# Performance work log

Measured on AMD Instinct MI355X. Metric: run time of the kernel, lower is better.

Reference implementation:

```python
import jax, jax.numpy as jnp
import numpy as np

H = 128
L = 3
G = 1024  # num graphs
BN_EPS = 1e-5


def _bn(h, gamma, beta):
    # BatchNorm1d in training mode: biased batch statistics over dim 0
    mu = jnp.mean(h, axis=0)
    var = jnp.var(h, axis=0)
    return (h - mu) * jax.lax.rsqrt(var + BN_EPS) * gamma + beta


def setup_inputs() -> dict:
    key = jax.random.key(0)
    ks = jax.random.split(key, 24)
    N, E, ND, ED = 100000, 1600000, 64, 16
    s = lambda k, shp: jax.random.normal(k, shp, dtype=jnp.float32) * 0.05
    inp = {
        "x": jax.random.normal(ks[0], (N, ND), dtype=jnp.float32),
        "edge_attr": jax.random.normal(ks[1], (E, ED), dtype=jnp.float32),
        "edge_index": jax.random.randint(ks[2], (2, E), 0, N, dtype=jnp.int32),
        "batch": jnp.sort(jax.random.randint(ks[3], (N,), 0, G, dtype=jnp.int32)),
        # embeddings
        "node_W": s(ks[4], (ND, H)), "node_b": jnp.zeros((H,), jnp.float32),
        "edge_W": s(ks[5], (ED, H)), "edge_b": jnp.zeros((H,), jnp.float32),
        # per-layer GINE MLP params (stacked over L layers)
        "W1s": s(ks[6], (L, H, 2 * H)), "b1s": jnp.zeros((L, 2 * H), jnp.float32),
        "g1s": jnp.ones((L, 2 * H), jnp.float32), "be1s": jnp.zeros((L, 2 * H), jnp.float32),
        "W2s": s(ks[7], (L, 2 * H, H)), "b2s": jnp.zeros((L, H), jnp.float32),
        "epss": jnp.zeros((L,), jnp.float32),  # train_eps=True, init 0
        # post-conv batchnorms
        "bn_g": jnp.ones((L, H), jnp.float32), "bn_b": jnp.zeros((L, H), jnp.float32),
        # readout
        "ro_W1": s(ks[8], (H, H)), "ro_b1": jnp.zeros((H,), jnp.float32),
        "ro_W2": s(ks[9], (H, H)), "ro_b2": jnp.zeros((H,), jnp.float32),
    }
    return inp


def reference(x, edge_attr, node_W, node_b, edge_W, edge_b, W1s, b1s, g1s, be1s,
              W2s, b2s, epss, bn_g, bn_b, ro_W1, ro_b1, ro_W2, ro_b2,
              edge_index, batch):
    N = x.shape[0]
    src, dst = edge_index[0], edge_index[1]
    h = x @ node_W + node_b                       # [N, H]
    e = edge_attr @ edge_W + edge_b               # [E, H]
    for i in range(L):
        # GINEConv: msg = relu(x_j + e), sum-aggregate at target
        msg = jax.nn.relu(h[src] + e)             # [E, H]
        aggr = jax.ops.segment_sum(msg, dst, num_segments=N)
        z = (1.0 + epss[i]) * h + aggr
        # nn: Linear -> BN -> ReLU -> Linear
        z = jax.nn.relu(_bn(z @ W1s[i] + b1s[i], g1s[i], be1s[i]))
        h = z @ W2s[i] + b2s[i]
        # outer BN + ReLU
        h = jax.nn.relu(_bn(h, bn_g[i], bn_b[i]))
    # global mean pool over graphs
    sums = jax.ops.segment_sum(h, batch, num_segments=G)
    cnts = jax.ops.segment_sum(jnp.ones((N,), h.dtype), batch, num_segments=G)
    pooled = sums / jnp.maximum(cnts, 1.0)[:, None]  # [G, H]
    emb = jax.nn.relu(pooled @ ro_W1 + ro_b1) @ ro_W2 + ro_b2
    return emb
```

## Files before the change

### kernel.cpp

```cpp
#include <hip/hip_runtime.h>


#define HCH 128
#define EDIM 16
#define NLAYER 3

typedef __attribute__((ext_vector_type(8))) short  s16x8;
typedef __attribute__((ext_vector_type(4))) float  f32x4;

static __device__ __forceinline__ float4 ld4(const float* p){
  return *reinterpret_cast<const float4*>(p);
}
static __device__ __forceinline__ float2 ld2(const float* p){
  return *reinterpret_cast<const float2*>(p);
}
static __device__ __forceinline__ unsigned short f2bf(float f){
  unsigned u = __float_as_uint(f);
  unsigned r = (u + 0x7FFFu + ((u >> 16) & 1u)) >> 16;
  return (unsigned short)r;
}
static __device__ __forceinline__ float bf2f(unsigned short h){
  return __uint_as_float(((unsigned)h) << 16);
}

__global__ void k_hist(const int* __restrict__ dst, int E, int* __restrict__ cnt){
  int j = blockIdx.x*blockDim.x + threadIdx.x;
  if (j < E) atomicAdd(&cnt[dst[j]], 1);
}

#define SC_T 256
#define SC_PER 8
#define SC_CHUNK (SC_T*SC_PER)

__global__ void k_scan1(const int* __restrict__ cnt, int N, int* __restrict__ bsum){
  __shared__ int sh[SC_T];
  int base = blockIdx.x*SC_CHUNK;
  int s = 0;
  #pragma unroll
  for (int u=0;u<SC_PER;++u){ int i = base + threadIdx.x*SC_PER + u; if (i<N) s += cnt[i]; }
  sh[threadIdx.x] = s; __syncthreads();
  for (int off=128; off>0; off>>=1){
    if (threadIdx.x < off) sh[threadIdx.x] += sh[threadIdx.x+off];
    __syncthreads();
  }
  if (threadIdx.x==0) bsum[blockIdx.x] = sh[0];
}

__global__ void k_scan2(const int* __restrict__ bsum, int NB, int* __restrict__ boff,
                        int* __restrict__ row_start, int N){
  if (threadIdx.x==0 && blockIdx.x==0){
    int run = 0;
    for (int b=0;b<NB;++b){ boff[b] = run; run += bsum[b]; }
    row_start[N] = run;
  }
}

__global__ void k_scan3(const int* __restrict__ cnt, int N, const int* __restrict__ boff,
                        int* __restrict__ row_start, int* __restrict__ cursor){
  __shared__ int sh[SC_T];
  int base = blockIdx.x*SC_CHUNK;
  int loc[SC_PER];
  int tsum = 0;
  #pragma unroll
  for (int u=0;u<SC_PER;++u){
    int i = base + threadIdx.x*SC_PER + u;
    int v = (i<N) ? cnt[i] : 0;
    loc[u] = v; tsum += v;
  }
  sh[threadIdx.x] = tsum; __syncthreads();
  for (int off=1; off<SC_T; off<<=1){
    int v = (threadIdx.x>=off) ? sh[threadIdx.x-off] : 0;
    __syncthreads();
    sh[threadIdx.x] += v;
    __syncthreads();
  }
  int run = boff[blockIdx.x] + sh[threadIdx.x] - tsum;
  #pragma unroll
  for (int u=0;u<SC_PER;++u){
    int i = base + threadIdx.x*SC_PER + u;
    if (i<N){ row_start[i] = run; cursor[i] = run; run += loc[u]; }
  }
}

__global__ void k_scatter(const int* __restrict__ src, const int* __restrict__ dst, int E,
                          int* __restrict__ cursor, int* __restrict__ perm,
                          int* __restrict__ src_perm){
  int j = blockIdx.x*blockDim.x + threadIdx.x;
  if (j < E){
    int d = dst[j];
    int pos = atomicAdd(&cursor[d], 1);
    perm[pos] = j;
    src_perm[pos] = src[j];
  }
}

__global__ void k_gather_attr(const int* __restrict__ perm, const float* __restrict__ edge_attr,
                              int E, float* __restrict__ attr_p){
  int t = blockIdx.x*blockDim.x + threadIdx.x;
  int e = t >> 2, f = t & 3;
  if (e < E){
    int j = perm[e];
    float4 v = ld4(edge_attr + (size_t)j*EDIM + f*4);
    *reinterpret_cast<float4*>(attr_p + (size_t)e*EDIM + f*4) = v;
  }
}

__global__ __launch_bounds__(256, 4) void k_msg8(
    const float* __restrict__ h, const float* __restrict__ attr_p,
    const float* __restrict__ edge_W, const float* __restrict__ edge_b,
    const int* __restrict__ row_start, const int* __restrict__ src_perm,
    int N, float* __restrict__ aggr){
  __shared__ float attr_lds[4][2][128];
  int tid = threadIdx.x;
  int wv = __builtin_amdgcn_readfirstlane(tid >> 6);
  int lane = tid & 63;
  int n = blockIdx.x*4 + wv;
  if (n >= N) return;
  int c = lane*2;
  float w0[EDIM], w1[EDIM];
  #pragma unroll
  for (int k=0;k<EDIM;++k){
    float2 w = ld2(edge_W + k*HCH + c);
    w0[k] = w.x; w1[k] = w.y;
  }
  float2 eb = ld2(edge_b + c);
  const float* hc = h + c;
  float a0 = 0.f, a1 = 0.f;
  int e0 = row_start[n], e1 = row_start[n+1];

  if (e0 < e1){
    int last = e1 - 1;
    int nb = (e1 - e0 + 7) >> 3;
    int le = lane >> 3;
    int lf = (lane & 7) * 2;
    float* ldsw = &attr_lds[wv][0][0];

    int sC[8], sN[8];
    #pragma unroll
    for (int j=0;j<8;++j){ int e=e0+j;   sC[j]=src_perm[e<last?e:last]; }
    #pragma unroll
    for (int j=0;j<8;++j){ int e=e0+8+j; sN[j]=src_perm[e<last?e:last]; }
    float2 HC[8];
    #pragma unroll
    for (int j=0;j<8;++j) HC[j] = ld2(hc + (size_t)sC[j]*HCH);
    int ea = e0 + le; ea = ea<last?ea:last;
    float2 atC = ld2(attr_p + (size_t)ea*EDIM + lf);

    for (int b=0; b<nb; ++b){
      int buf = (b & 1) * 128;
      *reinterpret_cast<float2*>(&ldsw[buf + le*16 + lf]) = atC;
      int ean = e0 + (b+1)*8 + le; ean = ean<last?ean:last;
      float2 atN = ld2(attr_p + (size_t)ean*EDIM + lf);
      float2 HN[8];
      #pragma unroll
      for (int j=0;j<8;++j) HN[j] = ld2(hc + (size_t)sN[j]*HCH);
      int sN2[8];
      #pragma unroll
      for (int j=0;j<8;++j){ int e=e0+(b+2)*8+j; sN2[j]=src_perm[e<last?e:last]; }
      int vcnt = e1 - (e0 + b*8);
      #pragma unroll
      for (int j=0;j<8;++j){
        const float* ap = &ldsw[buf + j*16];
        float4 t0 = *reinterpret_cast<const float4*>(ap);
        float4 t1 = *reinterpret_cast<const float4*>(ap+4);
        float4 t2 = *reinterpret_cast<const float4*>(ap+8);
        float4 t3 = *reinterpret_cast<const float4*>(ap+12);
        float m0 = eb.x, m1 = eb.y;
        m0 = fmaf(t0.x,w0[0],m0);  m1 = fmaf(t0.x,w1[0],m1);
        m0 = fmaf(t0.y,w0[1],m0);  m1 = fmaf(t0.y,w1[1],m1);
        m0 = fmaf(t0.z,w0[2],m0);  m1 = fmaf(t0.z,w1[2],m1);
        m0 = fmaf(t0.w,w0[3],m0);  m1 = fmaf(t0.w,w1[3],m1);
        m0 = fmaf(t1.x,w0[4],m0);  m1 = fmaf(t1.x,w1[4],m1);
        m0 = fmaf(t1.y,w0[5],m0);  m1 = fmaf(t1.y,w1[5],m1);
        m0 = fmaf(t1.z,w0[6],m0);  m1 = fmaf(t1.z,w1[6],m1);
        m0 = fmaf(t1.w,w0[7],m0);  m1 = fmaf(t1.w,w1[7],m1);
        m0 = fmaf(t2.x,w0[8],m0);  m1 = fmaf(t2.x,w1[8],m1);
        m0 = fmaf(t2.y,w0[9],m0);  m1 = fmaf(t2.y,w1[9],m1);
        m0 = fmaf(t2.z,w0[10],m0); m1 = fmaf(t2.z,w1[10],m1);
        m0 = fmaf(t2.w,w0[11],m0); m1 = fmaf(t2.w,w1[11],m1);
        m0 = fmaf(t3.x,w0[12],m0); m1 = fmaf(t3.x,w1[12],m1);
        m0 = fmaf(t3.y,w0[13],m0); m1 = fmaf(t3.y,w1[13],m1);
        m0 = fmaf(t3.z,w0[14],m0); m1 = fmaf(t3.z,w1[14],m1);
        m0 = fmaf(t3.w,w0[15],m0); m1 = fmaf(t3.w,w1[15],m1);
        float mj = (j < vcnt) ? 1.f : 0.f;
        a0 = fmaf(mj, fmaxf(m0 + HC[j].x, 0.f), a0);
        a1 = fmaf(mj, fmaxf(m1 + HC[j].y, 0.f), a1);
      }
      #pragma unroll
      for (int j=0;j<8;++j){ HC[j] = HN[j]; sN[j] = sN2[j]; }
      atC = atN;
    }
  }
  *reinterpret_cast<float2*>(aggr + (size_t)n*HCH + c) = make_float2(a0, a1);
}

__global__ void k_prepw(const float* __restrict__ W, int K, int M,
                        unsigned short* __restrict__ hi, unsigned short* __restrict__ lo){
  int t = blockIdx.x*blockDim.x + threadIdx.x;
  if (t < K*M){
    int m = t / K, k = t - m*K;
    float v = W[(size_t)k*M + m];
    unsigned short h = f2bf(v);
    hi[t] = h;
    lo[t] = f2bf(v - bf2f(h));
  }
}

enum { IN_PLAIN=0, IN_GINE=1, IN_BNRELU=2 };

template<int IN_MODE, bool STATS>
__global__ __launch_bounds__(256, 2) void k_mgemm(
    const float* __restrict__ A, const float* __restrict__ A2,
    const float* __restrict__ epsp,
    const float* __restrict__ bscale, const float* __restrict__ bshift,
    const unsigned short* __restrict__ Wthi, const unsigned short* __restrict__ Wtlo,
    const float* __restrict__ bias, float* __restrict__ C,
    float* __restrict__ sums, float* __restrict__ sumsq,
    int nrows, int K, int M){
  __shared__ __align__(16) short Zh[128*64];
  __shared__ __align__(16) short Zl[128*64];
  __shared__ __align__(16) short Bh[128*64];
  __shared__ __align__(16) short Bl[128*64];
  int tid = threadIdx.x;
  int rb = blockIdx.x*128, cb = blockIdx.y*128;
  int l = tid & 63, w = tid >> 6;
  int wrow = (w>>1)*64, wcol = (w&1)*64;

  f32x4 acc[4][4];
  #pragma unroll
  for (int fr=0; fr<4; ++fr)
    #pragma unroll
    for (int fc=0; fc<4; ++fc){ f32x4 z = {0.f,0.f,0.f,0.f}; acc[fr][fc] = z; }

  float epsv = 0.f;
  if (IN_MODE==IN_GINE) epsv = 1.0f + *epsp;

  int srow = tid >> 1, shalf = tid & 1;

  for (int k0 = 0; k0 < K; k0 += 64){
    {
      bool valid = (rb + srow) < nrows;
      const float* Ar  = A  + (size_t)(rb+srow)*K + k0;
      const float* A2r = (IN_MODE==IN_GINE) ? (A2 + (size_t)(rb+srow)*K + k0) : nullptr;
      #pragma unroll
      for (int s=0; s<4; ++s){
        int ko = (shalf*4 + s)*8;
        float v[8];
        if (valid){
          float4 u0 = ld4(Ar+ko), u1 = ld4(Ar+ko+4);
          v[0]=u0.x; v[1]=u0.y; v[2]=u0.z; v[3]=u0.w;
          v[4]=u1.x; v[5]=u1.y; v[6]=u1.z; v[7]=u1.w;
          if (IN_MODE==IN_GINE){
            float4 a0 = ld4(A2r+ko), a1 = ld4(A2r+ko+4);
            float a[8] = {a0.x,a0.y,a0.z,a0.w,a1.x,a1.y,a1.z,a1.w};
            #pragma unroll
            for (int j=0;j<8;++j) v[j] = fmaf(epsv, v[j], a[j]);
          } else if (IN_MODE==IN_BNRELU){
            float4 sc0 = ld4(bscale + k0+ko), sc1 = ld4(bscale + k0+ko+4);
            float4 sh0 = ld4(bshift + k0+ko), sh1 = ld4(bshift + k0+ko+4);
            float sc[8] = {sc0.x,sc0.y,sc0.z,sc0.w,sc1.x,sc1.y,sc1.z,sc1.w};
            float sh[8] = {sh0.x,sh0.y,sh0.z,sh0.w,sh1.x,sh1.y,sh1.z,sh1.w};
            #pragma unroll
            for (int j=0;j<8;++j) v[j] = fmaxf(fmaf(v[j], sc[j], sh[j]), 0.f);
          }
        } else {
          #pragma unroll
          for (int j=0;j<8;++j) v[j] = 0.f;
        }
        s16x8 hv, lv;
        #pragma unroll
        for (int j=0;j<8;++j){
          unsigned short hb = f2bf(v[j]);
          hv[j] = (short)hb;
          lv[j] = (short)f2bf(v[j] - bf2f(hb));
        }
        int idx = (srow*64 + ko) ^ ((srow&7)<<3);
        *reinterpret_cast<s16x8*>(&Zh[idx]) = hv;
        *reinterpret_cast<s16x8*>(&Zl[idx]) = lv;
      }
    }
    {
      const unsigned short* Wh = Wthi + (size_t)(cb+srow)*K + k0;
      const unsigned short* Wl = Wtlo + (size_t)(cb+srow)*K + k0;
      #pragma unroll
      for (int s=0; s<4; ++s){
        int ko = (shalf*4 + s)*8;
        s16x8 hv = *reinterpret_cast<const s16x8*>(Wh + ko);
        s16x8 lv = *reinterpret_cast<const s16x8*>(Wl + ko);
        int idx = (srow*64 + ko) ^ ((srow&7)<<3);
        *reinterpret_cast<s16x8*>(&Bh[idx]) = hv;
        *reinterpret_cast<s16x8*>(&Bl[idx]) = lv;
      }
    }
    __syncthreads();
    #pragma unroll
    for (int kc = 0; kc < 64; kc += 32){
      int kgo = kc + (l>>4)*8;
      s16x8 ah[4], al[4], bh[4], bl[4];
      #pragma unroll
      for (int f=0; f<4; ++f){
        int r = wrow + f*16 + (l&15);
        int ia = (r*64 + kgo) ^ ((r&7)<<3);
        ah[f] = *reinterpret_cast<const s16x8*>(&Zh[ia]);
        al[f] = *reinterpret_cast<const s16x8*>(&Zl[ia]);
        int cc = wcol + f*16 + (l&15);
        int ib = (cc*64 + kgo) ^ ((cc&7)<<3);
        bh[f] = *reinterpret_cast<const s16x8*>(&Bh[ib]);
        bl[f] = *reinterpret_cast<const s16x8*>(&Bl[ib]);
      }
      #pragma unroll
      for (int fr=0; fr<4; ++fr)
        #pragma unroll
        for (int fc=0; fc<4; ++fc){
          acc[fr][fc] = __builtin_amdgcn_mfma_f32_16x16x32_bf16(ah[fr], bh[fc], acc[fr][fc], 0,0,0);
          acc[fr][fc] = __builtin_amdgcn_mfma_f32_16x16x32_bf16(ah[fr], bl[fc], acc[fr][fc], 0,0,0);
          acc[fr][fc] = __builtin_amdgcn_mfma_f32_16x16x32_bf16(al[fr], bh[fc], acc[fr][fc], 0,0,0);
        }
    }
    __syncthreads();
  }
  float bv[4];
  #pragma unroll
  for (int fc=0; fc<4; ++fc) bv[fc] = bias[cb + wcol + fc*16 + (l&15)];
  float cs[4] = {0.f,0.f,0.f,0.f}, cq[4] = {0.f,0.f,0.f,0.f};
  int rbase = rb + wrow + (l>>4)*4;
  #pragma unroll
  for (int fr=0; fr<4; ++fr){
    #pragma unroll
    for (int r=0; r<4; ++r){
      int grow = rbase + fr*16 + r;
      if (grow < nrows){
        float* Cr = C + (size_t)grow*M + cb + wcol + (l&15);
        #pragma unroll
        for (int fc=0; fc<4; ++fc){
          float v = acc[fr][fc][r] + bv[fc];
          Cr[fc*16] = v;
          if (STATS){ cs[fc] += v; cq[fc] = fmaf(v, v, cq[fc]); }
        }
      }
    }
  }
  if (STATS){
    __syncthreads();
    float* S = reinterpret_cast<float*>(&Zh[0]);
    float* Q = S + 128;
    if (tid < 128){ S[tid] = 0.f; Q[tid] = 0.f; }
    __syncthreads();
    #pragma unroll
    for (int fc=0; fc<4; ++fc){
      atomicAdd(&S[wcol + fc*16 + (l&15)], cs[fc]);
      atomicAdd(&Q[wcol + fc*16 + (l&15)], cq[fc]);
    }
    __syncthreads();
    if (tid < 128){
      atomicAdd(&sums[cb + tid], S[tid]);
      atomicAdd(&sumsq[cb + tid], Q[tid]);
    }
  }
}

__global__ void k_finalize(const float* __restrict__ sums, const float* __restrict__ sumsq,
                           const float* __restrict__ gamma, const float* __restrict__ beta,
                           float invN, int C, float* __restrict__ scale,
                           float* __restrict__ shift){
  int c = blockIdx.x*blockDim.x + threadIdx.x;
  if (c < C){
    float mu  = sums[c]*invN;
    float var = sumsq[c]*invN - mu*mu;
    float rstd = rsqrtf(var + 1e-5f);
    float sc = gamma[c]*rstd;
    scale[c] = sc;
    shift[c] = beta[c] - mu*sc;
  }
}

__global__ void k_bnrelu(const float* __restrict__ h2, const float* __restrict__ scale,
                         const float* __restrict__ shift, int total4, float* __restrict__ h){
  int i = blockIdx.x*blockDim.x + threadIdx.x;
  if (i < total4){
    int c4 = (i & 31)*4;
    float4 v = reinterpret_cast<const float4*>(h2)[i];
    float4 sc = ld4(scale + c4), sh = ld4(shift + c4);
    v.x = fmaxf(fmaf(v.x, sc.x, sh.x), 0.f);
    v.y = fmaxf(fmaf(v.y, sc.y, sh.y), 0.f);
    v.z = fmaxf(fmaf(v.z, sc.z, sh.z), 0.f);
    v.w = fmaxf(fmaf(v.w, sc.w, sh.w), 0.f);
    reinterpret_cast<float4*>(h)[i] = v;
  }
}

__global__ void k_bounds(const int* __restrict__ batch, int N,
                         int* __restrict__ gstart, int* __restrict__ gend){
  int n = blockIdx.x*blockDim.x + threadIdx.x;
  if (n < N){
    int b = batch[n];
    if (n == 0) gstart[b] = 0;
    else { int pb = batch[n-1]; if (pb != b){ gstart[b] = n; gend[pb] = n; } }
    if (n == N-1) gend[b] = N;
  }
}

__global__ __launch_bounds__(128) void k_pool(const float* __restrict__ h,
                                              const int* __restrict__ gstart,
                                              const int* __restrict__ gend,
                                              float* __restrict__ pooled){
  int g = blockIdx.x, c = threadIdx.x;
  int s = gstart[g], e = gend[g];
  float acc = 0.f;
  for (int n = s; n < e; ++n) acc += h[(size_t)n*HCH + c];
  pooled[g*HCH + c] = (e > s) ? acc / (float)(e - s) : 0.f;
}

#define TR 128
#define BKC 64

template<bool OUT_RELU>
__global__ __launch_bounds__(256, 2) void k_gemm(
    const float* __restrict__ A,
    const float* __restrict__ W, const float* __restrict__ bias,
    float* __restrict__ C, int nrows, int K, int M){
  __shared__ __align__(16) float Zl2[TR][BKC+1];
  __shared__ __align__(16) float Wl[BKC][128];
  int tid = threadIdx.x;
  int ty = tid >> 4, tx = tid & 15;
  int rb = blockIdx.x * TR, cb = blockIdx.y * 128;
  float acc[8][8];
  #pragma unroll
  for (int j=0;j<8;++j)
    #pragma unroll
    for (int i=0;i<8;++i) acc[j][i] = 0.f;

  for (int k0 = 0; k0 < K; k0 += BKC){
    #pragma unroll
    for (int t=0;t<8;++t){
      int idx = t*256 + tid;
      int f4 = idx & 15, row = idx >> 4;
      int grow = rb + row, gk = k0 + f4*4;
      float4 v = make_float4(0.f,0.f,0.f,0.f);
      if (grow < nrows) v = ld4(A + (size_t)grow*K + gk);
      Zl2[row][f4*4+0] = v.x; Zl2[row][f4*4+1] = v.y;
      Zl2[row][f4*4+2] = v.z; Zl2[row][f4*4+3] = v.w;
    }
    #pragma unroll
    for (int t=0;t<8;++t){
      int idx = t*256 + tid;
      int f4 = idx & 31, kk = idx >> 5;
      float4 v = ld4(W + (size_t)(k0+kk)*M + cb + f4*4);
      *reinterpret_cast<float4*>(&Wl[kk][f4*4]) = v;
    }
    __syncthreads();
    #pragma unroll 4
    for (int k=0;k<BKC;++k){
      float zr[8], wr[8];
      #pragma unroll
      for (int j=0;j<8;++j) zr[j] = Zl2[ty+16*j][k];
      #pragma unroll
      for (int i=0;i<8;++i) wr[i] = Wl[k][tx+16*i];
      #pragma unroll
      for (int j=0;j<8;++j)
        #pragma unroll
        for (int i=0;i<8;++i) acc[j][i] = fmaf(zr[j], wr[i], acc[j][i]);
    }
    __syncthreads();
  }
  float bv[8];
  #pragma unroll
  for (int i=0;i<8;++i) bv[i] = bias[cb + tx + 16*i];
  #pragma unroll
  for (int j=0;j<8;++j){
    int grow = rb + ty + 16*j;
    if (grow < nrows){
      #pragma unroll
      for (int i=0;i<8;++i){
        float v = acc[j][i] + bv[i];
        if (OUT_RELU) v = fmaxf(v, 0.f);
        C[(size_t)grow*M + cb + tx + 16*i] = v;
      }
    }
  }
}

extern "C" void kernel_launch(void* const* d_in, const int* in_sizes, int n_in,
                              void* d_out, int out_size, void* d_ws, size_t ws_size,
                              hipStream_t stream){
  const float* x         = (const float*)d_in[0];
  const float* edge_attr = (const float*)d_in[1];
  const int*   edge_index= (const int*)  d_in[2];
  const int*   batch     = (const int*)  d_in[3];
  const float* node_W    = (const float*)d_in[4];
  const float* node_b    = (const float*)d_in[5];
  const float* edge_W    = (const float*)d_in[6];
  const float* edge_b    = (const float*)d_in[7];
  const float* W1s       = (const float*)d_in[8];
  const float* b1s       = (const float*)d_in[9];
  const float* g1s       = (const float*)d_in[10];
  const float* be1s      = (const float*)d_in[11];
  const float* W2s       = (const float*)d_in[12];
  const float* b2s       = (const float*)d_in[13];
  const float* epss      = (const float*)d_in[14];
  const float* bn_g      = (const float*)d_in[15];
  const float* bn_b      = (const float*)d_in[16];
  const float* ro_W1     = (const float*)d_in[17];
  const float* ro_b1     = (const float*)d_in[18];
  const float* ro_W2     = (const float*)d_in[19];
  const float* ro_b2     = (const float*)d_in[20];

  const int N = in_sizes[0] / 64;
  const int E = in_sizes[1] / EDIM;
  const int G = out_size / HCH;
  const int* src = edge_index;
  const int* dst = edge_index + E;

  char* p = (char*)d_ws;
  auto alloc = [&](size_t bytes)->char*{
    char* r = p; p += (bytes + 255) & ~(size_t)255; return r;
  };
  float* h       = (float*)alloc((size_t)N*HCH*4);
  float* aggr    = (float*)alloc((size_t)N*HCH*4);
  float* h2      = aggr;
  float* z1      = (float*)alloc((size_t)N*256*4);
  int*   cnt     = (int*)  alloc((size_t)N*4);
  int*   row_start=(int*)  alloc((size_t)(N+1)*4);
  int*   cursor  = (int*)  alloc((size_t)N*4);
  int*   perm    = (int*)  alloc((size_t)E*4);
  int*   src_perm= (int*)  alloc((size_t)E*4);
  int*   bsum    = (int*)  alloc(4096);
  int*   boff    = (int*)  alloc(4096);
  float* sums    = (float*)alloc(256*4);
  float* sumsq   = (float*)alloc(256*4);
  float* scale1  = (float*)alloc(256*4);
  float* shift1  = (float*)alloc(256*4);
  float* scale2  = (float*)alloc(128*4);
  float* shift2  = (float*)alloc(128*4);
  int*   gstart  = (int*)  alloc((size_t)G*4);
  int*   gend    = (int*)  alloc((size_t)G*4);
  float* pooled  = (float*)alloc((size_t)G*HCH*4);
  float* r1      = (float*)alloc((size_t)G*HCH*4);
  unsigned short* wtn_hi = (unsigned short*)alloc(128*64*2);
  unsigned short* wtn_lo = (unsigned short*)alloc(128*64*2);
  unsigned short* wt1_hi = (unsigned short*)alloc((size_t)NLAYER*256*128*2);
  unsigned short* wt1_lo = (unsigned short*)alloc((size_t)NLAYER*256*128*2);
  unsigned short* wt2_hi = (unsigned short*)alloc((size_t)NLAYER*128*256*2);
  unsigned short* wt2_lo = (unsigned short*)alloc((size_t)NLAYER*128*256*2);
  size_t used = (size_t)(p - (char*)d_ws);
  bool use_pre = (used + (size_t)E*EDIM*4 + 256) <= ws_size;
  float* attr_p  = use_pre ? (float*)alloc((size_t)E*EDIM*4) : nullptr;

  k_prepw<<<(64*128+255)/256, 256, 0, stream>>>(node_W, 64, 128, wtn_hi, wtn_lo);
  for (int l = 0; l < NLAYER; ++l){
    k_prepw<<<(128*256+255)/256, 256, 0, stream>>>(
        W1s + (size_t)l*128*256, 128, 256, wt1_hi + (size_t)l*32768, wt1_lo + (size_t)l*32768);
    k_prepw<<<(256*128+255)/256, 256, 0, stream>>>(
        W2s + (size_t)l*256*128, 256, 128, wt2_hi + (size_t)l*32768, wt2_lo + (size_t)l*32768);
  }

  hipMemsetAsync(cnt, 0, (size_t)N*4, stream);
  k_hist<<<(E+255)/256, 256, 0, stream>>>(dst, E, cnt);
  int NB = (N + SC_CHUNK - 1)/SC_CHUNK;
  k_scan1<<<NB, SC_T, 0, stream>>>(cnt, N, bsum);
  k_scan2<<<1, 64, 0, stream>>>(bsum, NB, boff, row_start, N);
  k_scan3<<<NB, SC_T, 0, stream>>>(cnt, N, boff, row_start, cursor);
  k_scatter<<<(E+255)/256, 256, 0, stream>>>(src, dst, E, cursor, perm, src_perm);
  if (use_pre)
    k_gather_attr<<<((size_t)E*4+255)/256, 256, 0, stream>>>(perm, edge_attr, E, attr_p);

  hipMemsetAsync(gstart, 0, (size_t)G*4, stream);
  hipMemsetAsync(gend,   0, (size_t)G*4, stream);
  k_bounds<<<(N+255)/256, 256, 0, stream>>>(batch, N, gstart, gend);

  const int NRB = (N + 127)/128;
  const float invN = 1.0f/(float)N;

  k_mgemm<IN_PLAIN,false><<<dim3(NRB,1), 256, 0, stream>>>(
      x, nullptr, nullptr, nullptr, nullptr, wtn_hi, wtn_lo, node_b, h,
      nullptr, nullptr, N, 64, 128);

  for (int l = 0; l < NLAYER; ++l){
    if (use_pre)
      k_msg8<<<(N+3)/4, 256, 0, stream>>>(h, attr_p, edge_W, edge_b,
                                          row_start, src_perm, N, aggr);
    else
      k_msg8<<<(N+3)/4, 256, 0, stream>>>(h, edge_attr, edge_W, edge_b,
                                          row_start, src_perm, N, aggr);
    hipMemsetAsync(sums,  0, 256*4, stream);
    hipMemsetAsync(sumsq, 0, 256*4, stream);
    k_mgemm<IN_GINE,true><<<dim3(NRB,2), 256, 0, stream>>>(
        h, aggr, epss + l, nullptr, nullptr,
        wt1_hi + (size_t)l*32768, wt1_lo + (size_t)l*32768,
        b1s + (size_t)l*256, z1, sums, sumsq, N, 128, 256);
    k_finalize<<<1, 256, 0, stream>>>(sums, sumsq, g1s + (size_t)l*256,
                                      be1s + (size_t)l*256, invN, 256, scale1, shift1);
    hipMemsetAsync(sums,  0, 128*4, stream);
    hipMemsetAsync(sumsq, 0, 128*4, stream);
    k_mgemm<IN_BNRELU,true><<<dim3(NRB,1), 256, 0, stream>>>(
        z1, nullptr, nullptr, scale1, shift1,
        wt2_hi + (size_t)l*32768, wt2_lo + (size_t)l*32768,
        b2s + (size_t)l*128, h2, sums, sumsq, N, 256, 128);
    k_finalize<<<1, 128, 0, stream>>>(sums, sumsq, bn_g + (size_t)l*128,
                                      bn_b + (size_t)l*128, invN, 128, scale2, shift2);
    int total4 = N * (HCH/4);
    k_bnrelu<<<(total4+255)/256, 256, 0, stream>>>(h2, scale2, shift2, total4, h);
  }

  k_pool<<<G, 128, 0, stream>>>(h, gstart, gend, pooled);
  dim3 gr((G + TR - 1)/TR, 1);
  k_gemm<true ><<<gr, 256, 0, stream>>>(pooled, ro_W1, ro_b1, r1, G, 128, 128);
  k_gemm<false><<<gr, 256, 0, stream>>>(r1, ro_W2, ro_b2, (float*)d_out, G, 128, 128);
}
```

Before: 1.731 ms.

## Fuse scatter with attr gather, fold BN finalize into consumers, packed FMA messages

```diff
diff --git a/kernel.cpp b/kernel.cpp
--- a/kernel.cpp
+++ b/kernel.cpp
@@ -7,12 +7,13 @@
 
 typedef __attribute__((ext_vector_type(8))) short  s16x8;
 typedef __attribute__((ext_vector_type(4))) float  f32x4;
+typedef __attribute__((ext_vector_type(2))) float  f32x2;
 
 static __device__ __forceinline__ float4 ld4(const float* p){
   return *reinterpret_cast<const float4*>(p);
 }
-static __device__ __forceinline__ float2 ld2(const float* p){
-  return *reinterpret_cast<const float2*>(p);
+static __device__ __forceinline__ f32x2 ld2v(const float* p){
+  return *reinterpret_cast<const f32x2*>(p);
 }
 static __device__ __forceinline__ unsigned short f2bf(float f){
   unsigned u = __float_as_uint(f);
@@ -82,26 +83,22 @@
   }
 }
 
-__global__ void k_scatter(const int* __restrict__ src, const int* __restrict__ dst, int E,
-                          int* __restrict__ cursor, int* __restrict__ perm,
-                          int* __restrict__ src_perm){
+__global__ void k_scatter2(const int* __restrict__ src, const int* __restrict__ dst,
+                           const float* __restrict__ edge_attr, int E,
+                           int* __restrict__ cursor, int* __restrict__ src_perm,
+                           float* __restrict__ attr_p){
   int j = blockIdx.x*blockDim.x + threadIdx.x;
   if (j < E){
     int d = dst[j];
     int pos = atomicAdd(&cursor[d], 1);
-    perm[pos] = j;
     src_perm[pos] = src[j];
-  }
-}
-
-__global__ void k_gather_attr(const int* __restrict__ perm, const float* __restrict__ edge_attr,
-                              int E, float* __restrict__ attr_p){
-  int t = blockIdx.x*blockDim.x + threadIdx.x;
-  int e = t >> 2, f = t & 3;
-  if (e < E){
-    int j = perm[e];
-    float4 v = ld4(edge_attr + (size_t)j*EDIM + f*4);
-    *reinterpret_cast<float4*>(attr_p + (size_t)e*EDIM + f*4) = v;
+    const float* ap = edge_attr + (size_t)j*EDIM;
+    float4 a0 = ld4(ap), a1 = ld4(ap+4), a2 = ld4(ap+8), a3 = ld4(ap+12);
+    float* op = attr_p + (size_t)pos*EDIM;
+    *reinterpret_cast<float4*>(op)    = a0;
+    *reinterpret_cast<float4*>(op+4)  = a1;
+    *reinterpret_cast<float4*>(op+8)  = a2;
+    *reinterpret_cast<float4*>(op+12) = a3;
   }
 }
 
@@ -117,13 +114,10 @@
   int n = blockIdx.x*4 + wv;
   if (n >= N) return;
   int c = lane*2;
-  float w0[EDIM], w1[EDIM];
-  #pragma unroll
-  for (int k=0;k<EDIM;++k){
-    float2 w = ld2(edge_W + k*HCH + c);
-    w0[k] = w.x; w1[k] = w.y;
-  }
-  float2 eb = ld2(edge_b + c);
+  f32x2 wp[16];
+  #pragma unroll
+  for (int k=0;k<16;++k) wp[k] = ld2v(edge_W + k*HCH + c);
+  f32x2 eb = ld2v(edge_b + c);
   const float* hc = h + c;
   float a0 = 0.f, a1 = 0.f;
   int e0 = row_start[n], e1 = row_start[n+1];
@@ -140,51 +134,39 @@
     for (int j=0;j<8;++j){ int e=e0+j;   sC[j]=src_perm[e<last?e:last]; }
     #pragma unroll
     for (int j=0;j<8;++j){ int e=e0+8+j; sN[j]=src_perm[e<last?e:last]; }
-    float2 HC[8];
-    #pragma unroll
-    for (int j=0;j<8;++j) HC[j] = ld2(hc + (size_t)sC[j]*HCH);
+    f32x2 HC[8];
+    #pragma unroll
+    for (int j=0;j<8;++j) HC[j] = ld2v(hc + (size_t)sC[j]*HCH);
     int ea = e0 + le; ea = ea<last?ea:last;
-    float2 atC = ld2(attr_p + (size_t)ea*EDIM + lf);
+    f32x2 atC = ld2v(attr_p + (size_t)ea*EDIM + lf);
 
     for (int b=0; b<nb; ++b){
       int buf = (b & 1) * 128;
-      *reinterpret_cast<float2*>(&ldsw[buf + le*16 + lf]) = atC;
+      *reinterpret_cast<f32x2*>(&ldsw[buf + le*16 + lf]) = atC;
       int ean = e0 + (b+1)*8 + le; ean = ean<last?ean:last;
-      float2 atN = ld2(attr_p + (size_t)ean*EDIM + lf);
-      float2 HN[8];
-      #pragma unroll
-      for (int j=0;j<8;++j) HN[j] = ld2(hc + (size_t)sN[j]*HCH);
+      f32x2 atN = ld2v(attr_p + (size_t)ean*EDIM + lf);
+      f32x2 HN[8];
+      #pragma unroll
+      for (int j=0;j<8;++j) HN[j] = ld2v(hc + (size_t)sN[j]*HCH);
       int sN2[8];
       #pragma unroll
       for (int j=0;j<8;++j){ int e=e0+(b+2)*8+j; sN2[j]=src_perm[e<last?e:last]; }
       int vcnt = e1 - (e0 + b*8);
       #pragma unroll
       for (int j=0;j<8;++j){
-        const float* ap = &ldsw[buf + j*16];
-        float4 t0 = *reinterpret_cast<const float4*>(ap);
-        float4 t1 = *reinterpret_cast<const float4*>(ap+4);
-        float4 t2 = *reinterpret_cast<const float4*>(ap+8);
-        float4 t3 = *reinterpret_cast<const float4*>(ap+12);
-        float m0 = eb.x, m1 = eb.y;
-        m0 = fmaf(t0.x,w0[0],m0);  m1 = fmaf(t0.x,w1[0],m1);
-        m0 = fmaf(t0.y,w0[1],m0);  m1 = fmaf(t0.y,w1[1],m1);
-        m0 = fmaf(t0.z,w0[2],m0);  m1 = fmaf(t0.z,w1[2],m1);
-        m0 = fmaf(t0.w,w0[3],m0);  m1 = fmaf(t0.w,w1[3],m1);
-        m0 = fmaf(t1.x,w0[4],m0);  m1 = fmaf(t1.x,w1[4],m1);
-        m0 = fmaf(t1.y,w0[5],m0);  m1 = fmaf(t1.y,w1[5],m1);
-        m0 = fmaf(t1.z,w0[6],m0);  m1 = fmaf(t1.z,w1[6],m1);
-        m0 = fmaf(t1.w,w0[7],m0);  m1 = fmaf(t1.w,w1[7],m1);
-        m0 = fmaf(t2.x,w0[8],m0);  m1 = fmaf(t2.x,w1[8],m1);
-        m0 = fmaf(t2.y,w0[9],m0);  m1 = fmaf(t2.y,w1[9],m1);
-        m0 = fmaf(t2.z,w0[10],m0); m1 = fmaf(t2.z,w1[10],m1);
-        m0 = fmaf(t2.w,w0[11],m0); m1 = fmaf(t2.w,w1[11],m1);
-        m0 = fmaf(t3.x,w0[12],m0); m1 = fmaf(t3.x,w1[12],m1);
-        m0 = fmaf(t3.y,w0[13],m0); m1 = fmaf(t3.y,w1[13],m1);
-        m0 = fmaf(t3.z,w0[14],m0); m1 = fmaf(t3.z,w1[14],m1);
-        m0 = fmaf(t3.w,w0[15],m0); m1 = fmaf(t3.w,w1[15],m1);
+        const f32x2* ap2 = reinterpret_cast<const f32x2*>(&ldsw[buf + j*16]);
+        f32x2 m = eb;
+        #pragma unroll
+        for (int i=0;i<8;++i){
+          f32x2 t = ap2[i];
+          asm("v_pk_fma_f32 %0, %1, %2, %0 op_sel:[0,0,0] op_sel_hi:[1,0,1]"
+              : "+v"(m) : "v"(wp[2*i]), "v"(t));
+          asm("v_pk_fma_f32 %0, %1, %2, %0 op_sel:[0,1,0] op_sel_hi:[1,1,1]"
+              : "+v"(m) : "v"(wp[2*i+1]), "v"(t));
+        }
         float mj = (j < vcnt) ? 1.f : 0.f;
-        a0 = fmaf(mj, fmaxf(m0 + HC[j].x, 0.f), a0);
-        a1 = fmaf(mj, fmaxf(m1 + HC[j].y, 0.f), a1);
+        a0 = fmaf(mj, fmaxf(m[0] + HC[j][0], 0.f), a0);
+        a1 = fmaf(mj, fmaxf(m[1] + HC[j][1], 0.f), a1);
       }
       #pragma unroll
       for (int j=0;j<8;++j){ HC[j] = HN[j]; sN[j] = sN2[j]; }
@@ -194,16 +176,29 @@
   *reinterpret_cast<float2*>(aggr + (size_t)n*HCH + c) = make_float2(a0, a1);
 }
 
-__global__ void k_prepw(const float* __restrict__ W, int K, int M,
-                        unsigned short* __restrict__ hi, unsigned short* __restrict__ lo){
+__global__ void k_prepall(const float* __restrict__ node_W,
+                          const float* __restrict__ W1s, const float* __restrict__ W2s,
+                          unsigned short* __restrict__ wtn_hi, unsigned short* __restrict__ wtn_lo,
+                          unsigned short* __restrict__ wt1_hi, unsigned short* __restrict__ wt1_lo,
+                          unsigned short* __restrict__ wt2_hi, unsigned short* __restrict__ wt2_lo){
   int t = blockIdx.x*blockDim.x + threadIdx.x;
-  if (t < K*M){
-    int m = t / K, k = t - m*K;
-    float v = W[(size_t)k*M + m];
-    unsigned short h = f2bf(v);
-    hi[t] = h;
-    lo[t] = f2bf(v - bf2f(h));
-  }
+  const float* src; unsigned short *hi, *lo; int K, M, idx;
+  if (t < 8192){
+    src = node_W; hi = wtn_hi; lo = wtn_lo; K = 64; M = 128; idx = t;
+  } else if (t < 8192 + 3*32768){
+    int u = t - 8192; int l = u >> 15; idx = u & 32767;
+    src = W1s + (size_t)l*32768; hi = wt1_hi + (size_t)l*32768; lo = wt1_lo + (size_t)l*32768;
+    K = 128; M = 256;
+  } else if (t < 8192 + 6*32768){
+    int u = t - 8192 - 3*32768; int l = u >> 15; idx = u & 32767;
+    src = W2s + (size_t)l*32768; hi = wt2_hi + (size_t)l*32768; lo = wt2_lo + (size_t)l*32768;
+    K = 256; M = 128;
+  } else return;
+  int m = idx / K, k = idx - m*K;
+  float v = src[(size_t)k*M + m];
+  unsigned short hb = f2bf(v);
+  hi[idx] = hb;
+  lo[idx] = f2bf(v - bf2f(hb));
 }
 
 enum { IN_PLAIN=0, IN_GINE=1, IN_BNRELU=2 };
@@ -212,15 +207,17 @@
 __global__ __launch_bounds__(256, 2) void k_mgemm(
     const float* __restrict__ A, const float* __restrict__ A2,
     const float* __restrict__ epsp,
-    const float* __restrict__ bscale, const float* __restrict__ bshift,
+    const float* __restrict__ sums_in, const float* __restrict__ sumsq_in,
+    const float* __restrict__ gamma, const float* __restrict__ beta, float invN,
     const unsigned short* __restrict__ Wthi, const unsigned short* __restrict__ Wtlo,
     const float* __restrict__ bias, float* __restrict__ C,
-    float* __restrict__ sums, float* __restrict__ sumsq,
+    float* __restrict__ sums_out, float* __restrict__ sumsq_out,
     int nrows, int K, int M){
   __shared__ __align__(16) short Zh[128*64];
   __shared__ __align__(16) short Zl[128*64];
   __shared__ __align__(16) short Bh[128*64];
   __shared__ __align__(16) short Bl[128*64];
+  __shared__ float scl[64], shf[64];
   int tid = threadIdx.x;
   int rb = blockIdx.x*128, cb = blockIdx.y*128;
   int l = tid & 63, w = tid >> 6;
@@ -238,6 +235,18 @@
   int srow = tid >> 1, shalf = tid & 1;
 
   for (int k0 = 0; k0 < K; k0 += 64){
+    if (IN_MODE==IN_BNRELU){
+      if (tid < 64){
+        int kk = k0 + tid;
+        float mu  = sums_in[kk]*invN;
+        float var = sumsq_in[kk]*invN - mu*mu;
+        float rstd = rsqrtf(var + 1e-5f);
+        float sc = gamma[kk]*rstd;
+        scl[tid] = sc;
+        shf[tid] = beta[kk] - mu*sc;
+      }
+      __syncthreads();
+    }
     {
       bool valid = (rb + srow) < nrows;
       const float* Ar  = A  + (size_t)(rb+srow)*K + k0;
@@ -256,12 +265,8 @@
             #pragma unroll
             for (int j=0;j<8;++j) v[j] = fmaf(epsv, v[j], a[j]);
           } else if (IN_MODE==IN_BNRELU){
-            float4 sc0 = ld4(bscale + k0+ko), sc1 = ld4(bscale + k0+ko+4);
-            float4 sh0 = ld4(bshift + k0+ko), sh1 = ld4(bshift + k0+ko+4);
-            float sc[8] = {sc0.x,sc0.y,sc0.z,sc0.w,sc1.x,sc1.y,sc1.z,sc1.w};
-            float sh[8] = {sh0.x,sh0.y,sh0.z,sh0.w,sh1.x,sh1.y,sh1.z,sh1.w};
             #pragma unroll
-            for (int j=0;j<8;++j) v[j] = fmaxf(fmaf(v[j], sc[j], sh[j]), 0.f);
+            for (int j=0;j<8;++j) v[j] = fmaxf(fmaf(v[j], scl[ko+j], shf[ko+j]), 0.f);
           }
         } else {
           #pragma unroll
@@ -353,38 +358,34 @@
     }
     __syncthreads();
     if (tid < 128){
-      atomicAdd(&sums[cb + tid], S[tid]);
-      atomicAdd(&sumsq[cb + tid], Q[tid]);
-    }
-  }
-}
-
-__global__ void k_finalize(const float* __restrict__ sums, const float* __restrict__ sumsq,
-                           const float* __restrict__ gamma, const float* __restrict__ beta,
-                           float invN, int C, float* __restrict__ scale,
-                           float* __restrict__ shift){
-  int c = blockIdx.x*blockDim.x + threadIdx.x;
-  if (c < C){
-    float mu  = sums[c]*invN;
-    float var = sumsq[c]*invN - mu*mu;
-    float rstd = rsqrtf(var + 1e-5f);
-    float sc = gamma[c]*rstd;
-    scale[c] = sc;
-    shift[c] = beta[c] - mu*sc;
-  }
-}
-
-__global__ void k_bnrelu(const float* __restrict__ h2, const float* __restrict__ scale,
-                         const float* __restrict__ shift, int total4, float* __restrict__ h){
+      atomicAdd(&sums_out[cb + tid], S[tid]);
+      atomicAdd(&sumsq_out[cb + tid], Q[tid]);
+    }
+  }
+}
+
+__global__ void k_bnrelu(const float* __restrict__ h2,
+                         const float* __restrict__ sums, const float* __restrict__ sumsq,
+                         const float* __restrict__ gamma, const float* __restrict__ beta,
+                         float invN, int total4, float* __restrict__ h){
   int i = blockIdx.x*blockDim.x + threadIdx.x;
   if (i < total4){
     int c4 = (i & 31)*4;
     float4 v = reinterpret_cast<const float4*>(h2)[i];
-    float4 sc = ld4(scale + c4), sh = ld4(shift + c4);
-    v.x = fmaxf(fmaf(v.x, sc.x, sh.x), 0.f);
-    v.y = fmaxf(fmaf(v.y, sc.y, sh.y), 0.f);
-    v.z = fmaxf(fmaf(v.z, sc.z, sh.z), 0.f);
-    v.w = fmaxf(fmaf(v.w, sc.w, sh.w), 0.f);
+    float sc[4], sh[4];
+    #pragma unroll
+    for (int t=0;t<4;++t){
+      int cc = c4 + t;
+      float mu  = sums[cc]*invN;
+      float var = sumsq[cc]*invN - mu*mu;
+      float rstd = rsqrtf(var + 1e-5f);
+      float s = gamma[cc]*rstd;
+      sc[t] = s; sh[t] = beta[cc] - mu*s;
+    }
+    v.x = fmaxf(fmaf(v.x, sc[0], sh[0]), 0.f);
+    v.y = fmaxf(fmaf(v.y, sc[1], sh[1]), 0.f);
+    v.z = fmaxf(fmaf(v.z, sc[2], sh[2]), 0.f);
+    v.w = fmaxf(fmaf(v.w, sc[3], sh[3]), 0.f);
     reinterpret_cast<float4*>(h)[i] = v;
   }
 }
@@ -522,16 +523,12 @@
   int*   cnt     = (int*)  alloc((size_t)N*4);
   int*   row_start=(int*)  alloc((size_t)(N+1)*4);
   int*   cursor  = (int*)  alloc((size_t)N*4);
-  int*   perm    = (int*)  alloc((size_t)E*4);
   int*   src_perm= (int*)  alloc((size_t)E*4);
   int*   bsum    = (int*)  alloc(4096);
   int*   boff    = (int*)  alloc(4096);
-  float* sums    = (float*)alloc(256*4);
-  float* sumsq   = (float*)alloc(256*4);
-  float* scale1  = (float*)alloc(256*4);
-  float* shift1  = (float*)alloc(256*4);
-  float* scale2  = (float*)alloc(128*4);
-  float* shift2  = (float*)alloc(128*4);
+  float* stat    = (float*)alloc(1024*4);
+  float* statA   = stat;
+  float* statB   = stat + 512;
   int*   gstart  = (int*)  alloc((size_t)G*4);
   int*   gend    = (int*)  alloc((size_t)G*4);
   float* pooled  = (float*)alloc((size_t)G*HCH*4);
@@ -542,17 +539,10 @@
   unsigned short* wt1_lo = (unsigned short*)alloc((size_t)NLAYER*256*128*2);
   unsigned short* wt2_hi = (unsigned short*)alloc((size_t)NLAYER*128*256*2);
   unsigned short* wt2_lo = (unsigned short*)alloc((size_t)NLAYER*128*256*2);
-  size_t used = (size_t)(p - (char*)d_ws);
-  bool use_pre = (used + (size_t)E*EDIM*4 + 256) <= ws_size;
-  float* attr_p  = use_pre ? (float*)alloc((size_t)E*EDIM*4) : nullptr;
-
-  k_prepw<<<(64*128+255)/256, 256, 0, stream>>>(node_W, 64, 128, wtn_hi, wtn_lo);
-  for (int l = 0; l < NLAYER; ++l){
-    k_prepw<<<(128*256+255)/256, 256, 0, stream>>>(
-        W1s + (size_t)l*128*256, 128, 256, wt1_hi + (size_t)l*32768, wt1_lo + (size_t)l*32768);
-    k_prepw<<<(256*128+255)/256, 256, 0, stream>>>(
-        W2s + (size_t)l*256*128, 256, 128, wt2_hi + (size_t)l*32768, wt2_lo + (size_t)l*32768);
-  }
+  float* attr_p  = (float*)alloc((size_t)E*EDIM*4);
+
+  k_prepall<<<800, 256, 0, stream>>>(node_W, W1s, W2s,
+                                     wtn_hi, wtn_lo, wt1_hi, wt1_lo, wt2_hi, wt2_lo);
 
   hipMemsetAsync(cnt, 0, (size_t)N*4, stream);
   k_hist<<<(E+255)/256, 256, 0, stream>>>(dst, E, cnt);
@@ -560,46 +550,36 @@
   k_scan1<<<NB, SC_T, 0, stream>>>(cnt, N, bsum);
   k_scan2<<<1, 64, 0, stream>>>(bsum, NB, boff, row_start, N);
   k_scan3<<<NB, SC_T, 0, stream>>>(cnt, N, boff, row_start, cursor);
-  k_scatter<<<(E+255)/256, 256, 0, stream>>>(src, dst, E, cursor, perm, src_perm);
-  if (use_pre)
-    k_gather_attr<<<((size_t)E*4+255)/256, 256, 0, stream>>>(perm, edge_attr, E, attr_p);
-
-  hipMemsetAsync(gstart, 0, (size_t)G*4, stream);
-  hipMemsetAsync(gend,   0, (size_t)G*4, stream);
+  k_scatter2<<<(E+255)/256, 256, 0, stream>>>(src, dst, edge_attr, E,
+                                              cursor, src_perm, attr_p);
+
+  hipMemsetAsync(gstart, 0, (size_t)2*G*4, stream);
   k_bounds<<<(N+255)/256, 256, 0, stream>>>(batch, N, gstart, gend);
 
   const int NRB = (N + 127)/128;
   const float invN = 1.0f/(float)N;
 
   k_mgemm<IN_PLAIN,false><<<dim3(NRB,1), 256, 0, stream>>>(
-      x, nullptr, nullptr, nullptr, nullptr, wtn_hi, wtn_lo, node_b, h,
-      nullptr, nullptr, N, 64, 128);
+      x, nullptr, nullptr, nullptr, nullptr, nullptr, nullptr, 0.f,
+      wtn_hi, wtn_lo, node_b, h, nullptr, nullptr, N, 64, 128);
 
   for (int l = 0; l < NLAYER; ++l){
-    if (use_pre)
-      k_msg8<<<(N+3)/4, 256, 0, stream>>>(h, attr_p, edge_W, edge_b,
-                                          row_start, src_perm, N, aggr);
-    else
-      k_msg8<<<(N+3)/4, 256, 0, stream>>>(h, edge_attr, edge_W, edge_b,
-                                          row_start, src_perm, N, aggr);
-    hipMemsetAsync(sums,  0, 256*4, stream);
-    hipMemsetAsync(sumsq, 0, 256*4, stream);
+    k_msg8<<<(N+3)/4, 256, 0, stream>>>(h, attr_p, edge_W, edge_b,
+                                        row_start, src_perm, N, aggr);
+    hipMemsetAsync(stat, 0, 1024*4, stream);
     k_mgemm<IN_GINE,true><<<dim3(NRB,2), 256, 0, stream>>>(
-        h, aggr, epss + l, nullptr, nullptr,
+        h, aggr, epss + l, nullptr, nullptr, nullptr, nullptr, invN,
         wt1_hi + (size_t)l*32768, wt1_lo + (size_t)l*32768,
-        b1s + (size_t)l*256, z1, sums, sumsq, N, 128, 256);
-    k_finalize<<<1, 256, 0, stream>>>(sums, sumsq, g1s + (size_t)l*256,
-                                      be1s + (size_t)l*256, invN, 256, scale1, shift1);
-    hipMemsetAsync(sums,  0, 128*4, stream);
-    hipMemsetAsync(sumsq, 0, 128*4, stream);
+        b1s + (size_t)l*256, z1, statA, statA + 256, N, 128, 256);
     k_mgemm<IN_BNRELU,true><<<dim3(NRB,1), 256, 0, stream>>>(
-        z1, nullptr, nullptr, scale1, shift1,
+        z1, nullptr, nullptr, statA, statA + 256,
+        g1s + (size_t)l*256, be1s + (size_t)l*256, invN,
         wt2_hi + (size_t)l*32768, wt2_lo + (size_t)l*32768,
-        b2s + (size_t)l*128, h2, sums, sumsq, N, 256, 128);
-    k_finalize<<<1, 128, 0, stream>>>(sums, sumsq, bn_g + (size_t)l*128,
-                                      bn_b + (size_t)l*128, invN, 128, scale2, shift2);
+        b2s + (size_t)l*128, h2, statB, statB + 256, N, 256, 128);
     int total4 = N * (HCH/4);
-    k_bnrelu<<<(total4+255)/256, 256, 0, stream>>>(h2, scale2, shift2, total4, h);
+    k_bnrelu<<<(total4+255)/256, 256, 0, stream>>>(
+        h2, statB, statB + 256, bn_g + (size_t)l*128, bn_b + (size_t)l*128,
+        invN, total4, h);
   }
 
   k_pool<<<G, 128, 0, stream>>>(h, gstart, gend, pooled);
```

Result: faster. 1.691 ms (-2.3%).
